# Kernel tuning notes

Hardware: AMD Instinct MI355X
Metric: run time of the kernel (lower is better)

Reference implementation:

```python
import jax, jax.numpy as jnp
import numpy as np

NUM_ITEM = 80000
NUM_USER = 20000
N = NUM_ITEM + NUM_USER
E = 1_000_000
DIM_FEAT = 64
USER_DIM = 128
DIM_ID = 64
SLOPE = 0.01  # F.leaky_relu default negative_slope


def setup_inputs() -> dict:
    key = jax.random.key(0)
    ks = jax.random.split(key, 16)
    s = 0.05
    # self-loop-free random edge list (torch code removes self loops)
    src = jax.random.randint(ks[0], (E,), 0, N)
    off = jax.random.randint(ks[1], (E,), 1, N)
    dst = (src + off) % N
    edge_index = jnp.stack([src, dst]).astype(jnp.int32)
    return {
        "features": jax.random.normal(ks[2], (NUM_ITEM, DIM_FEAT), jnp.float32),
        "user_features": jax.random.normal(ks[3], (NUM_USER, USER_DIM), jnp.float32),
        "id_embedding_weight": jax.random.normal(ks[4], (N, DIM_ID), jnp.float32) * s,
        "user_mlp_w": jax.random.normal(ks[5], (DIM_FEAT, USER_DIM), jnp.float32) * s,
        "user_mlp_b": jnp.zeros((DIM_FEAT,), jnp.float32),
        "gat1_w": jax.random.normal(ks[6], (DIM_FEAT, DIM_FEAT), jnp.float32) * s,
        "lin1_w": jax.random.normal(ks[7], (DIM_ID, DIM_FEAT), jnp.float32) * s,
        "lin1_b": jnp.zeros((DIM_ID,), jnp.float32),
        "g1_w": jax.random.normal(ks[8], (DIM_ID, DIM_FEAT), jnp.float32) * s,
        "g1_b": jnp.zeros((DIM_ID,), jnp.float32),
        "gat2_w": jax.random.normal(ks[9], (DIM_ID, DIM_ID), jnp.float32) * s,
        "lin2_w": jax.random.normal(ks[10], (DIM_ID, DIM_ID), jnp.float32) * s,
        "lin2_b": jnp.zeros((DIM_ID,), jnp.float32),
        "g2_w": jax.random.normal(ks[11], (DIM_ID, DIM_ID), jnp.float32) * s,
        "g2_b": jnp.zeros((DIM_ID,), jnp.float32),
        "edge_index": edge_index,
    }


def leaky_relu(x):
    return jnp.where(x >= 0, x, SLOPE * x)


def graph_gat(x, W, src, dst):
    """GraphGAT layer (MGAT-style): x@W, inner-product attention with
    degree-based sigmoid gate, edge softmax over target nodes, scatter-add."""
    n = x.shape[0]
    xw = x @ W                                   # [N, d_out]
    x_i = xw[dst]                                # gathered target feats [E, d]
    x_j = xw[src]                                # gathered source feats [E, d]
    inner = jnp.sum(x_i * x_j, axis=-1)          # [E]
    deg = jnp.zeros((n,), xw.dtype).at[src].add(1.0)
    dinv = deg[src] ** -0.5                      # deg[src] >= 1 by construction
    gate = jax.nn.sigmoid(dinv * inner)
    logits = inner * gate
    # segment softmax over destination index (PyG softmax)
    m = jax.ops.segment_max(logits, dst, num_segments=n)
    m = jnp.where(jnp.isfinite(m), m, 0.0)
    e = jnp.exp(logits - m[dst])
    z = jax.ops.segment_sum(e, dst, num_segments=n)
    attn = e / (z[dst] + 1e-16)
    msg = x_j * attn[:, None]                    # [E, d]
    return jnp.zeros_like(xw).at[dst].add(msg)   # scatter-add aggr


def reference(features, user_features, id_embedding_weight,
              user_mlp_w, user_mlp_b,
              gat1_w, lin1_w, lin1_b, g1_w, g1_b,
              gat2_w, lin2_w, lin2_b, g2_w, g2_b,
              edge_index):
    src, dst = edge_index[0], edge_index[1]
    user = jnp.tanh(user_features @ user_mlp_w.T + user_mlp_b)
    x = jnp.concatenate([features, user], axis=0)          # [N, dim_feat]
    nrm = jnp.linalg.norm(x, axis=-1, keepdims=True)
    x = x / jnp.maximum(nrm, 1e-12)                        # F.normalize

    # hop 1
    h = leaky_relu(graph_gat(x, gat1_w, src, dst))
    x_hat = leaky_relu(x @ lin1_w.T + lin1_b) + id_embedding_weight
    x1 = leaky_relu(h @ g1_w.T + g1_b + x_hat)

    # hop 2
    h = leaky_relu(graph_gat(x1, gat2_w, src, dst))
    x_hat = leaky_relu(x1 @ lin2_w.T + lin2_b) + id_embedding_weight
    x2 = leaky_relu(h @ g2_w.T + g2_b + x_hat)

    return jnp.concatenate([x1, x2], axis=1)               # [N, 2*dim_id]
```

## Files before the change

kernel.cpp:

```cpp
#include <hip/hip_runtime.h>
#include <hip/hip_bf16.h>

#define N_ITEM 80000
#define N_USER 20000
#define NN     100000
#define NE     1000000
#define SCAN_T 1024
#define SCAN_TILES ((NN + SCAN_T - 1) / SCAN_T)

typedef __hip_bfloat16 bf16;

__device__ __forceinline__ float b2f(bf16 v) { return __bfloat162float(v); }
__device__ __forceinline__ bf16  f2b(float v) { return __float2bfloat16(v); }
__device__ __forceinline__ float bits2f(unsigned short h) {
    return __uint_as_float(((unsigned)h) << 16);
}
__device__ __forceinline__ float leaky(float v) { return v >= 0.f ? v : 0.01f * v; }

template<typename T>
__device__ __forceinline__ float ldT(const void* p, size_t i);
template<> __device__ __forceinline__ float ldT<float>(const void* p, size_t i) {
    return ((const float*)p)[i];
}
template<> __device__ __forceinline__ float ldT<bf16>(const void* p, size_t i) {
    return b2f(((const bf16*)p)[i]);
}
template<typename T>
__device__ __forceinline__ float4 ldT4(const void* p, size_t i);
template<> __device__ __forceinline__ float4 ldT4<float>(const void* p, size_t i) {
    return *(const float4*)((const float*)p + i);
}
template<> __device__ __forceinline__ float4 ldT4<bf16>(const void* p, size_t i) {
    ushort4 u = *(const ushort4*)((const unsigned short*)p + i);
    return make_float4(bits2f(u.x), bits2f(u.y), bits2f(u.z), bits2f(u.w));
}
template<typename T>
__device__ __forceinline__ void stT4(void* p, size_t i, float4 v);
template<> __device__ __forceinline__ void stT4<float>(void* p, size_t i, float4 v) {
    *(float4*)((float*)p + i) = v;
}
template<> __device__ __forceinline__ void stT4<bf16>(void* p, size_t i, float4 v) {
    bf16 b0 = f2b(v.x), b1 = f2b(v.y), b2 = f2b(v.z), b3 = f2b(v.w);
    ushort4 u = make_ushort4(*(unsigned short*)&b0, *(unsigned short*)&b1,
                             *(unsigned short*)&b2, *(unsigned short*)&b3);
    *(ushort4*)((unsigned short*)p + i) = u;
}
__device__ __forceinline__ float4 ld4f(const float* p, size_t i) {
    return *(const float4*)(p + i);
}
__device__ __forceinline__ float4 ld4b(const unsigned short* p, size_t i) {
    ushort4 u = *(const ushort4*)(p + i);
    return make_float4(bits2f(u.x), bits2f(u.y), bits2f(u.z), bits2f(u.w));
}
__device__ __forceinline__ void st4b(unsigned short* p, size_t i, float4 v) {
    bf16 b0 = f2b(v.x), b1 = f2b(v.y), b2 = f2b(v.z), b3 = f2b(v.w);
    ushort4 u = make_ushort4(*(unsigned short*)&b0, *(unsigned short*)&b1,
                             *(unsigned short*)&b2, *(unsigned short*)&b3);
    *(ushort4*)(p + i) = u;
}

__device__ __forceinline__ float wred(float v) {
    for (int o = 32; o; o >>= 1) v += __shfl_xor(v, o, 64);
    return v;
}
__device__ __forceinline__ float gred16(float v) {
    for (int o = 8; o; o >>= 1) v += __shfl_xor(v, o, 64);
    return v;
}
__device__ __forceinline__ int wscan(int v, int lane) {
    for (int o = 1; o < 64; o <<= 1) {
        int t = __shfl_up(v, o, 64);
        v += (lane >= o) ? t : 0;
    }
    return v;
}

__global__ void k_detect(const unsigned short* __restrict__ w, int* __restrict__ mode) {
    __shared__ int cnt[256];
    int bad = 0;
    for (int i = threadIdx.x; i < 4096; i += 256) {
        unsigned e = (w[i] >> 7) & 0xFFu;
        bad += (e == 0u || e == 0xFFu) ? 1 : 0;
    }
    cnt[threadIdx.x] = bad;
    __syncthreads();
    if (threadIdx.x == 0) {
        int t = 0;
        for (int k = 0; k < 256; k++) t += cnt[k];
        mode[0] = (t > 0) ? 1 : 0;
    }
}

__global__ void k_prep_w(const void* umw, const void* lw1, const void* gw1,
                         const void* lw2, const void* gw2,
                         float* umwT, float* wT, const int* mode) {
    int t = blockIdx.x * 256 + threadIdx.x;
    bool f32m = (*mode != 0);
    if (t < 8192) {
        int j = t >> 7, k = t & 127;
        float v = f32m ? ldT<float>(umw, t) : ldT<bf16>(umw, t);
        umwT[k * 64 + j] = v;
    } else {
        int u = t - 8192;
        int m = u >> 12;
        int r = u & 4095;
        int j = r >> 6, k = r & 63;
        const void* srcp = (m == 0) ? lw1 : (m == 1) ? gw1 : (m == 2) ? lw2 : gw2;
        float v = f32m ? ldT<float>(srcp, r) : ldT<bf16>(srcp, r);
        wT[m * 4096 + k * 64 + j] = v;
    }
}

__global__ void k_deg(const int* __restrict__ src, const int* __restrict__ dst,
                      int* __restrict__ deg, int* __restrict__ cnt) {
    int e = blockIdx.x * blockDim.x + threadIdx.x;
    if (e < NE) {
        atomicAdd(&deg[src[e]], 1);
        atomicAdd(&cnt[dst[e]], 1);
    }
}

__global__ void k_dinv(const int* __restrict__ deg, float* __restrict__ dinv) {
    int i = blockIdx.x * blockDim.x + threadIdx.x;
    if (i < NN) dinv[i] = rsqrtf((float)max(deg[i], 1));
}

__global__ void k_scan_sum(const int* __restrict__ cnt, int* __restrict__ tsum) {
    __shared__ int wsum[16];
    int i = blockIdx.x * SCAN_T + threadIdx.x;
    int lane = threadIdx.x & 63, wid = threadIdx.x >> 6;
    int v = (i < NN) ? cnt[i] : 0;
    float s = wred((float)v);
    if (lane == 0) wsum[wid] = (int)s;
    __syncthreads();
    if (threadIdx.x == 0) {
        int t = 0;
        #pragma unroll
        for (int k = 0; k < 16; k++) t += wsum[k];
        tsum[blockIdx.x] = t;
    }
}

__global__ void k_scan_tiles(const int* __restrict__ tsum, int* __restrict__ toff) {
    __shared__ int wsum[16];
    int lane = threadIdx.x & 63, wid = threadIdx.x >> 6;
    int v = (threadIdx.x < SCAN_TILES) ? tsum[threadIdx.x] : 0;
    int inc = wscan(v, lane);
    if (lane == 63) wsum[wid] = inc;
    __syncthreads();
    if (wid == 0) {
        int ws = (lane < 16) ? wsum[lane] : 0;
        int wi = wscan(ws, lane);
        if (lane < 16) wsum[lane] = wi - ws;
    }
    __syncthreads();
    if (threadIdx.x < SCAN_TILES) toff[threadIdx.x] = inc - v + wsum[wid];
}

__global__ void k_scan_out(const int* __restrict__ cnt, const int* __restrict__ toff,
                           int* __restrict__ csr_off, int* __restrict__ cursor) {
    __shared__ int wsum[16];
    int i = blockIdx.x * SCAN_T + threadIdx.x;
    int lane = threadIdx.x & 63, wid = threadIdx.x >> 6;
    int v = (i < NN) ? cnt[i] : 0;
    int inc = wscan(v, lane);
    if (lane == 63) wsum[wid] = inc;
    __syncthreads();
    if (wid == 0) {
        int ws = (lane < 16) ? wsum[lane] : 0;
        int wi = wscan(ws, lane);
        if (lane < 16) wsum[lane] = wi - ws;
    }
    __syncthreads();
    int excl = inc - v + wsum[wid] + toff[blockIdx.x];
    if (i < NN) { csr_off[i] = excl; cursor[i] = excl; }
    if (i == NN - 1) csr_off[NN] = excl + v;
}

__global__ void k_scatter(const int* __restrict__ src, const int* __restrict__ dst,
                          int* __restrict__ cursor, int* __restrict__ csr_src) {
    int e = blockIdx.x * blockDim.x + threadIdx.x;
    if (e < NE) {
        int pos = atomicAdd(&cursor[dst[e]], 1);
        csr_src[pos] = src[e];
    }
}

template<typename T>
__device__ __forceinline__ void prep_items_body(const void* feat, float* x) {
    int i = blockIdx.x * 4 + (threadIdx.x >> 6);
    int j = threadIdx.x & 63;
    if (i >= N_ITEM) return;
    float v = ldT<T>(feat, (size_t)i * 64 + j);
    float ss = wred(v * v);
    float inv = 1.f / fmaxf(sqrtf(ss), 1e-12f);
    x[(size_t)i * 64 + j] = v * inv;
}
__global__ void k_prep_items(const void* feat, float* x, const int* mode) {
    if (*mode) prep_items_body<float>(feat, x);
    else       prep_items_body<bf16>(feat, x);
}

template<typename T>
__device__ __forceinline__ void prep_users_body(const void* uf, const float* wT,
                                                const void* b, float* x) {
    int u = blockIdx.x * 4 + (threadIdx.x >> 6);
    int j = threadIdx.x & 63;
    if (u >= N_USER) return;
    size_t ub = (size_t)u * 128;
    float acc = ldT<T>(b, j);
    #pragma unroll 8
    for (int k = 0; k < 128; k++)
        acc += ldT<T>(uf, ub + k) * wT[k * 64 + j];
    float v = tanhf(acc);
    float ss = wred(v * v);
    float inv = 1.f / fmaxf(sqrtf(ss), 1e-12f);
    x[(size_t)(N_ITEM + u) * 64 + j] = v * inv;
}
__global__ void k_prep_users(const void* uf, const float* wT, const void* b,
                             float* x, const int* mode) {
    if (*mode) prep_users_body<float>(uf, wT, b, x);
    else       prep_users_body<bf16>(uf, wT, b, x);
}

template<typename T>
__device__ __forceinline__ void xw_body(const float* __restrict__ xin,
                                        const void* __restrict__ W,
                                        unsigned short* __restrict__ xw) {
    int lane = threadIdx.x & 63, wid = threadIdx.x >> 6;
    int sl = lane & 15;
    int i = blockIdx.x * 16 + (wid << 2) + (lane >> 4);
    if (i >= NN) return;
    size_t rb = (size_t)i * 64 + sl * 4;
    float4 xv = ld4f(xin, rb);
    float4 acc = make_float4(0.f, 0.f, 0.f, 0.f);
    int gbase = lane & 48;
    #pragma unroll
    for (int kk = 0; kk < 16; kk++) {
        int srcl = gbase | kk;
        float xb[4];
        xb[0] = __shfl(xv.x, srcl, 64);
        xb[1] = __shfl(xv.y, srcl, 64);
        xb[2] = __shfl(xv.z, srcl, 64);
        xb[3] = __shfl(xv.w, srcl, 64);
        #pragma unroll
        for (int q = 0; q < 4; q++) {
            float4 w4 = ldT4<T>(W, (size_t)(kk * 4 + q) * 64 + sl * 4);
            acc.x += xb[q] * w4.x; acc.y += xb[q] * w4.y;
            acc.z += xb[q] * w4.z; acc.w += xb[q] * w4.w;
        }
    }
    st4b(xw, rb, acc);
}
__global__ void k_xw(const float* xin, const void* W, unsigned short* xw,
                     const int* mode) {
    if (*mode) xw_body<float>(xin, W, xw);
    else       xw_body<bf16>(xin, W, xw);
}

template<typename T>
__device__ __forceinline__ void gat_body(const unsigned short* __restrict__ xw,
                                         const float* __restrict__ xin,
                                         const int* __restrict__ csr_off,
                                         const int* __restrict__ csr_src,
                                         const float* __restrict__ dinv,
                                         const float* __restrict__ gT, const void* gb,
                                         const float* __restrict__ lT, const void* lb,
                                         const void* id_emb,
                                         float* __restrict__ xnext, void* out,
                                         int off_out) {
    int lane = threadIdx.x & 63, wid = threadIdx.x >> 6;
    int sl = lane & 15;
    int i = blockIdx.x * 16 + (wid << 2) + (lane >> 4);
    if (i >= NN) return;
    size_t rb = (size_t)i * 64 + sl * 4;
    float4 xd = ld4b(xw, rb);
    int e0 = csr_off[i], e1 = csr_off[i + 1];
    int cnt = e1 - e0;
    float m = -1e30f, l = 0.f;
    float4 acc = make_float4(0.f, 0.f, 0.f, 0.f);
    float4 xsA = make_float4(0.f, 0.f, 0.f, 0.f), xsB = xsA;
    float dA = 1.f, dB = 1.f;
    if (cnt > 0) {
        int s0 = csr_src[e0];
        xsA = ld4b(xw, (size_t)s0 * 64 + sl * 4);
        dA = dinv[s0];
    }
    if (cnt > 1) {
        int s1 = csr_src[e0 + 1];
        xsB = ld4b(xw, (size_t)s1 * 64 + sl * 4);
        dB = dinv[s1];
    }
    for (int t = 0; t < cnt; ++t) {
        float4 xs = xsA; float dv = dA;
        xsA = xsB; dA = dB;
        if (t + 2 < cnt) {
            int sn = csr_src[e0 + t + 2];
            xsB = ld4b(xw, (size_t)sn * 64 + sl * 4);
            dB = dinv[sn];
        }
        float p = xd.x * xs.x + xd.y * xs.y + xd.z * xs.z + xd.w * xs.w;
        float inner = gred16(p);
        float gate = 1.f / (1.f + __expf(-dv * inner));
        float logit = inner * gate;
        float mn = fmaxf(m, logit);
        float sc = __expf(m - mn);
        float w  = __expf(logit - mn);
        acc.x = acc.x * sc + w * xs.x;
        acc.y = acc.y * sc + w * xs.y;
        acc.z = acc.z * sc + w * xs.z;
        acc.w = acc.w * sc + w * xs.w;
        l = l * sc + w;
        m = mn;
    }
    float linv = 1.f / (l + 1e-16f);
    float4 hv = make_float4(leaky(acc.x * linv), leaky(acc.y * linv),
                            leaky(acc.z * linv), leaky(acc.w * linv));
    float4 xv = ld4f(xin, rb);
    float4 accg = make_float4(0.f, 0.f, 0.f, 0.f);
    float4 accl = make_float4(0.f, 0.f, 0.f, 0.f);
    int gbase = lane & 48;
    #pragma unroll
    for (int kk = 0; kk < 16; kk++) {
        int srcl = gbase | kk;
        float hb[4], xb[4];
        hb[0] = __shfl(hv.x, srcl, 64); xb[0] = __shfl(xv.x, srcl, 64);
        hb[1] = __shfl(hv.y, srcl, 64); xb[1] = __shfl(xv.y, srcl, 64);
        hb[2] = __shfl(hv.z, srcl, 64); xb[2] = __shfl(xv.z, srcl, 64);
        hb[3] = __shfl(hv.w, srcl, 64); xb[3] = __shfl(xv.w, srcl, 64);
        #pragma unroll
        for (int q = 0; q < 4; q++) {
            size_t wb = (size_t)(kk * 4 + q) * 64 + sl * 4;
            float4 g4 = ld4f(gT, wb);
            float4 l4 = ld4f(lT, wb);
            accg.x += hb[q] * g4.x; accg.y += hb[q] * g4.y;
            accg.z += hb[q] * g4.z; accg.w += hb[q] * g4.w;
            accl.x += xb[q] * l4.x; accl.y += xb[q] * l4.y;
            accl.z += xb[q] * l4.z; accl.w += xb[q] * l4.w;
        }
    }
    float4 lb4 = ldT4<T>(lb, sl * 4);
    float4 gb4 = ldT4<T>(gb, sl * 4);
    float4 id4 = ldT4<T>(id_emb, rb);
    float4 xn;
    xn.x = leaky(accg.x + gb4.x + leaky(accl.x + lb4.x) + id4.x);
    xn.y = leaky(accg.y + gb4.y + leaky(accl.y + lb4.y) + id4.y);
    xn.z = leaky(accg.z + gb4.z + leaky(accl.z + lb4.z) + id4.z);
    xn.w = leaky(accg.w + gb4.w + leaky(accl.w + lb4.w) + id4.w);
    *(float4*)(xnext + rb) = xn;
    stT4<T>(out, (size_t)i * 128 + off_out + sl * 4, xn);
}
__global__ void k_gat(const unsigned short* xw, const float* xin,
                      const int* csr_off, const int* csr_src, const float* dinv,
                      const float* gT, const void* gb,
                      const float* lT, const void* lb, const void* id_emb,
                      float* xnext, void* out, int off_out, const int* mode) {
    if (*mode) gat_body<float>(xw, xin, csr_off, csr_src, dinv, gT, gb, lT, lb,
                               id_emb, xnext, out, off_out);
    else       gat_body<bf16>(xw, xin, csr_off, csr_src, dinv, gT, gb, lT, lb,
                              id_emb, xnext, out, off_out);
}

extern "C" void kernel_launch(void* const* d_in, const int* in_sizes, int n_in,
                              void* d_out, int out_size, void* d_ws, size_t ws_size,
                              hipStream_t stream) {
    const void* feat   = d_in[0];
    const void* uf     = d_in[1];
    const void* id_emb = d_in[2];
    const void* umw    = d_in[3];
    const void* umb    = d_in[4];
    const void* gat1   = d_in[5];
    const void* lin1b  = d_in[7];
    const void* g1b    = d_in[9];
    const void* gat2   = d_in[10];
    const void* lin2b  = d_in[12];
    const void* g2b    = d_in[14];
    const int*  ei     = (const int*)d_in[15];
    const int* src = ei;
    const int* dst = ei + NE;

    int*      mode   = (int*)d_ws;
    int*      deg    = (int*)((char*)d_ws + 16);
    int*      cnt    = deg + NN;
    int*      cursor = cnt + NN;
    int*      csr_off = cursor + NN;
    int*      tsum   = csr_off + NN + 16;
    int*      toff   = tsum + 128;
    float*    dinv   = (float*)(toff + 128);
    float*    umwT   = dinv + NN;
    float*    wT     = umwT + 8192;
    int*      csr_src = (int*)(wT + 4 * 4096);
    float*    buf0   = (float*)(csr_src + NE);
    float*    buf2   = buf0 + (size_t)NN * 64;
    unsigned short* xwb = (unsigned short*)(buf2 + (size_t)NN * 64);

    k_detect<<<1, 256, 0, stream>>>((const unsigned short*)feat, mode);
    k_prep_w<<<96, 256, 0, stream>>>(umw, d_in[6], d_in[8], d_in[11], d_in[13],
                                     umwT, wT, mode);
    hipMemsetAsync(deg, 0, 2 * NN * 4, stream);
    k_deg<<<(NE + 255) / 256, 256, 0, stream>>>(src, dst, deg, cnt);
    k_dinv<<<(NN + 255) / 256, 256, 0, stream>>>(deg, dinv);
    k_scan_sum<<<SCAN_TILES, SCAN_T, 0, stream>>>(cnt, tsum);
    k_scan_tiles<<<1, SCAN_T, 0, stream>>>(tsum, toff);
    k_scan_out<<<SCAN_TILES, SCAN_T, 0, stream>>>(cnt, toff, csr_off, cursor);
    k_scatter<<<(NE + 255) / 256, 256, 0, stream>>>(src, dst, cursor, csr_src);
    k_prep_items<<<(N_ITEM + 3) / 4, 256, 0, stream>>>(feat, buf0, mode);
    k_prep_users<<<(N_USER + 3) / 4, 256, 0, stream>>>(uf, umwT, umb, buf0, mode);

    const float* lT1 = wT;
    const float* gT1 = wT + 4096;
    const float* lT2 = wT + 8192;
    const float* gT2 = wT + 12288;

    int gat_blocks = (NN + 15) / 16;

    k_xw<<<gat_blocks, 256, 0, stream>>>(buf0, gat1, xwb, mode);
    k_gat<<<gat_blocks, 256, 0, stream>>>(xwb, buf0, csr_off, csr_src, dinv,
                                          gT1, g1b, lT1, lin1b, id_emb,
                                          buf2, d_out, 0, mode);
    k_xw<<<gat_blocks, 256, 0, stream>>>(buf2, gat2, xwb, mode);
    k_gat<<<gat_blocks, 256, 0, stream>>>(xwb, buf2, csr_off, csr_src, dinv,
                                          gT2, g2b, lT2, lin2b, id_emb,
                                          buf0, d_out, 64, mode);
}
```

Before: 680.5 us.

## Drop online-softmax max tracking and prefetch four edges ahead in GAT gather

Replaces the online softmax (running max with rescaling) by direct exp-sum accumulation, which removes two exps and the rescale work per edge. It also deepens the software prefetch of neighbour features from two to four edges, keeping more gathers in flight. The trade-off is a risk of exp overflow if logits are large; with normalized inputs and small weights they are expected to stay bounded.

After: 699.6 us. 1.03x slower.

```diff
diff --git a/kernel.cpp b/kernel.cpp
--- a/kernel.cpp
+++ b/kernel.cpp
@@ -277,42 +277,42 @@
     float4 xd = ld4b(xw, rb);
     int e0 = csr_off[i], e1 = csr_off[i + 1];
     int cnt = e1 - e0;
-    float m = -1e30f, l = 0.f;
+    float l = 0.f;
     float4 acc = make_float4(0.f, 0.f, 0.f, 0.f);
-    float4 xsA = make_float4(0.f, 0.f, 0.f, 0.f), xsB = xsA;
-    float dA = 1.f, dB = 1.f;
-    if (cnt > 0) {
-        int s0 = csr_src[e0];
-        xsA = ld4b(xw, (size_t)s0 * 64 + sl * 4);
-        dA = dinv[s0];
-    }
-    if (cnt > 1) {
-        int s1 = csr_src[e0 + 1];
-        xsB = ld4b(xw, (size_t)s1 * 64 + sl * 4);
-        dB = dinv[s1];
-    }
-    for (int t = 0; t < cnt; ++t) {
-        float4 xs = xsA; float dv = dA;
-        xsA = xsB; dA = dB;
-        if (t + 2 < cnt) {
-            int sn = csr_src[e0 + t + 2];
-            xsB = ld4b(xw, (size_t)sn * 64 + sl * 4);
-            dB = dinv[sn];
-        }
-        float p = xd.x * xs.x + xd.y * xs.y + xd.z * xs.z + xd.w * xs.w;
-        float inner = gred16(p);
-        float gate = 1.f / (1.f + __expf(-dv * inner));
-        float logit = inner * gate;
-        float mn = fmaxf(m, logit);
-        float sc = __expf(m - mn);
-        float w  = __expf(logit - mn);
-        acc.x = acc.x * sc + w * xs.x;
-        acc.y = acc.y * sc + w * xs.y;
-        acc.z = acc.z * sc + w * xs.z;
-        acc.w = acc.w * sc + w * xs.w;
-        l = l * sc + w;
-        m = mn;
-    }
+
+    float4 xs0 = make_float4(0.f, 0.f, 0.f, 0.f);
+    float4 xs1 = xs0, xs2 = xs0, xs3 = xs0;
+    float d0v = 1.f, d1v = 1.f, d2v = 1.f, d3v = 1.f;
+
+#define LOADE(XS, DV, IDX) { int s_ = csr_src[e0 + (IDX)]; \
+        XS = ld4b(xw, (size_t)s_ * 64 + sl * 4); DV = dinv[s_]; }
+#define PROC(XS, DV) { \
+        float p_ = xd.x * XS.x + xd.y * XS.y + xd.z * XS.z + xd.w * XS.w; \
+        float inner_ = gred16(p_); \
+        float gate_ = 1.f / (1.f + __expf(-(DV) * inner_)); \
+        float w_ = __expf(inner_ * gate_); \
+        acc.x += w_ * XS.x; acc.y += w_ * XS.y; \
+        acc.z += w_ * XS.z; acc.w += w_ * XS.w; \
+        l += w_; }
+
+    if (cnt > 0) LOADE(xs0, d0v, 0);
+    if (cnt > 1) LOADE(xs1, d1v, 1);
+    if (cnt > 2) LOADE(xs2, d2v, 2);
+    if (cnt > 3) LOADE(xs3, d3v, 3);
+    int t = 0;
+    for (; t + 4 <= cnt; t += 4) {
+        PROC(xs0, d0v); if (t + 4 < cnt) LOADE(xs0, d0v, t + 4);
+        PROC(xs1, d1v); if (t + 5 < cnt) LOADE(xs1, d1v, t + 5);
+        PROC(xs2, d2v); if (t + 6 < cnt) LOADE(xs2, d2v, t + 6);
+        PROC(xs3, d3v); if (t + 7 < cnt) LOADE(xs3, d3v, t + 7);
+    }
+    if (t     < cnt) PROC(xs0, d0v);
+    if (t + 1 < cnt) PROC(xs1, d1v);
+    if (t + 2 < cnt) PROC(xs2, d2v);
+    if (t + 3 < cnt) PROC(xs3, d3v);
+#undef LOADE
+#undef PROC
+
     float linv = 1.f / (l + 1e-16f);
     float4 hv = make_float4(leaky(acc.x * linv), leaky(acc.y * linv),
                             leaky(acc.z * linv), leaky(acc.w * linv));
```

## Assign one wavefront per node and split edges across four lane groups

Applied to the files above, without the earlier changes.

The GAT aggregation now uses a full 64-lane wave per destination node, with four 16-lane groups processing different edges concurrently and combining partial sums via xor shuffles. The online-softmax max tracking is removed in favour of a direct exp-sum, and the dense g/lin projections are split across groups with a cross-group reduction. This shortens the serial per-node edge loop and reduces intra-wave divergence from uneven degrees, at the cost of 4x more waves, extra shuffle reductions, and loss of overflow protection in the softmax.

Result: slower. 778.1 us (+14.3%).

```diff
diff --git a/kernel.cpp b/kernel.cpp
--- a/kernel.cpp
+++ b/kernel.cpp
@@ -270,48 +270,55 @@
                                          float* __restrict__ xnext, void* out,
                                          int off_out) {
     int lane = threadIdx.x & 63, wid = threadIdx.x >> 6;
-    int sl = lane & 15;
-    int i = blockIdx.x * 16 + (wid << 2) + (lane >> 4);
+    int sl = lane & 15, sub = lane >> 4;
+    int i = blockIdx.x * 4 + wid;
     if (i >= NN) return;
     size_t rb = (size_t)i * 64 + sl * 4;
     float4 xd = ld4b(xw, rb);
     int e0 = csr_off[i], e1 = csr_off[i + 1];
     int cnt = e1 - e0;
-    float m = -1e30f, l = 0.f;
+    int nb = (cnt + 3) >> 2;
+    float l = 0.f;
     float4 acc = make_float4(0.f, 0.f, 0.f, 0.f);
+
     float4 xsA = make_float4(0.f, 0.f, 0.f, 0.f), xsB = xsA;
-    float dA = 1.f, dB = 1.f;
-    if (cnt > 0) {
-        int s0 = csr_src[e0];
-        xsA = ld4b(xw, (size_t)s0 * 64 + sl * 4);
-        dA = dinv[s0];
-    }
-    if (cnt > 1) {
-        int s1 = csr_src[e0 + 1];
-        xsB = ld4b(xw, (size_t)s1 * 64 + sl * 4);
-        dB = dinv[s1];
-    }
-    for (int t = 0; t < cnt; ++t) {
-        float4 xs = xsA; float dv = dA;
-        xsA = xsB; dA = dB;
-        if (t + 2 < cnt) {
-            int sn = csr_src[e0 + t + 2];
-            xsB = ld4b(xw, (size_t)sn * 64 + sl * 4);
-            dB = dinv[sn];
+    float dA = 1.f, dB = 1.f, aA = 0.f, aB = 0.f;
+    if (nb > 0) {
+        int q = sub;
+        int s_ = csr_src[e0 + min(q, cnt - 1)];
+        xsA = ld4b(xw, (size_t)s_ * 64 + sl * 4); dA = dinv[s_];
+        aA = (q < cnt) ? 1.f : 0.f;
+    }
+    if (nb > 1) {
+        int q = 4 + sub;
+        int s_ = csr_src[e0 + min(q, cnt - 1)];
+        xsB = ld4b(xw, (size_t)s_ * 64 + sl * 4); dB = dinv[s_];
+        aB = (q < cnt) ? 1.f : 0.f;
+    }
+    for (int b = 0; b < nb; ++b) {
+        float4 xs = xsA; float dv = dA; float am = aA;
+        xsA = xsB; dA = dB; aA = aB;
+        if (b + 2 < nb) {
+            int q = (b + 2) * 4 + sub;
+            int s_ = csr_src[e0 + min(q, cnt - 1)];
+            xsB = ld4b(xw, (size_t)s_ * 64 + sl * 4); dB = dinv[s_];
+            aB = (q < cnt) ? 1.f : 0.f;
         }
         float p = xd.x * xs.x + xd.y * xs.y + xd.z * xs.z + xd.w * xs.w;
         float inner = gred16(p);
         float gate = 1.f / (1.f + __expf(-dv * inner));
-        float logit = inner * gate;
-        float mn = fmaxf(m, logit);
-        float sc = __expf(m - mn);
-        float w  = __expf(logit - mn);
-        acc.x = acc.x * sc + w * xs.x;
-        acc.y = acc.y * sc + w * xs.y;
-        acc.z = acc.z * sc + w * xs.z;
-        acc.w = acc.w * sc + w * xs.w;
-        l = l * sc + w;
-        m = mn;
+        float w = am * __expf(inner * gate);
+        acc.x += w * xs.x; acc.y += w * xs.y;
+        acc.z += w * xs.z; acc.w += w * xs.w;
+        l += w;
+    }
+    #pragma unroll
+    for (int o = 16; o <= 32; o <<= 1) {
+        acc.x += __shfl_xor(acc.x, o, 64);
+        acc.y += __shfl_xor(acc.y, o, 64);
+        acc.z += __shfl_xor(acc.z, o, 64);
+        acc.w += __shfl_xor(acc.w, o, 64);
+        l     += __shfl_xor(l, o, 64);
     }
     float linv = 1.f / (l + 1e-16f);
     float4 hv = make_float4(leaky(acc.x * linv), leaky(acc.y * linv),
@@ -319,10 +326,11 @@
     float4 xv = ld4f(xin, rb);
     float4 accg = make_float4(0.f, 0.f, 0.f, 0.f);
     float4 accl = make_float4(0.f, 0.f, 0.f, 0.f);
-    int gbase = lane & 48;
+    int gb16 = lane & 48;
     #pragma unroll
-    for (int kk = 0; kk < 16; kk++) {
-        int srcl = gbase | kk;
+    for (int kt = 0; kt < 4; kt++) {
+        int kk = sub * 4 + kt;
+        int srcl = gb16 | kk;
         float hb[4], xb[4];
         hb[0] = __shfl(hv.x, srcl, 64); xb[0] = __shfl(xv.x, srcl, 64);
         hb[1] = __shfl(hv.y, srcl, 64); xb[1] = __shfl(xv.y, srcl, 64);
@@ -339,6 +347,17 @@
             accl.z += xb[q] * l4.z; accl.w += xb[q] * l4.w;
         }
     }
+    #pragma unroll
+    for (int o = 16; o <= 32; o <<= 1) {
+        accg.x += __shfl_xor(accg.x, o, 64);
+        accg.y += __shfl_xor(accg.y, o, 64);
+        accg.z += __shfl_xor(accg.z, o, 64);
+        accg.w += __shfl_xor(accg.w, o, 64);
+        accl.x += __shfl_xor(accl.x, o, 64);
+        accl.y += __shfl_xor(accl.y, o, 64);
+        accl.z += __shfl_xor(accl.z, o, 64);
+        accl.w += __shfl_xor(accl.w, o, 64);
+    }
     float4 lb4 = ldT4<T>(lb, sl * 4);
     float4 gb4 = ldT4<T>(gb, sl * 4);
     float4 id4 = ldT4<T>(id_emb, rb);
@@ -347,8 +366,8 @@
     xn.y = leaky(accg.y + gb4.y + leaky(accl.y + lb4.y) + id4.y);
     xn.z = leaky(accg.z + gb4.z + leaky(accl.z + lb4.z) + id4.z);
     xn.w = leaky(accg.w + gb4.w + leaky(accl.w + lb4.w) + id4.w);
-    *(float4*)(xnext + rb) = xn;
-    stT4<T>(out, (size_t)i * 128 + off_out + sl * 4, xn);
+    if (sub == 0) *(float4*)(xnext + rb) = xn;
+    if (sub == 1) stT4<T>(out, (size_t)i * 128 + off_out + sl * 4, xn);
 }
 __global__ void k_gat(const unsigned short* xw, const float* xin,
                       const int* csr_off, const int* csr_src, const float* dinv,
@@ -412,13 +431,14 @@
     const float* lT2 = wT + 8192;
     const float* gT2 = wT + 12288;
 
-    int gat_blocks = (NN + 15) / 16;
-
-    k_xw<<<gat_blocks, 256, 0, stream>>>(buf0, gat1, xwb, mode);
+    int xw_blocks  = (NN + 15) / 16;
+    int gat_blocks = (NN + 3) / 4;
+
+    k_xw<<<xw_blocks, 256, 0, stream>>>(buf0, gat1, xwb, mode);
     k_gat<<<gat_blocks, 256, 0, stream>>>(xwb, buf0, csr_off, csr_src, dinv,
                                           gT1, g1b, lT1, lin1b, id_emb,
                                           buf2, d_out, 0, mode);
-    k_xw<<<gat_blocks, 256, 0, stream>>>(buf2, gat2, xwb, mode);
+    k_xw<<<xw_blocks, 256, 0, stream>>>(buf2, gat2, xwb, mode);
     k_gat<<<gat_blocks, 256, 0, stream>>>(xwb, buf2, csr_off, csr_src, dinv,
                                           gT2, g2b, lT2, lin2b, id_emb,
                                           buf0, d_out, 64, mode);
```

## Move lin branch into pre-GAT kernel, cache g-weights in LDS, skip final xnext

Applied to the files above, without the earlier changes.

Moves the x@lin^T + bias + leaky + id_embedding computation out of the GAT aggregation kernel into the x@W kernel, which writes it as an fp16 intermediate. The GAT kernel then only does the g-projection, reading its 64x64 weight from shared memory loaded once per block. The second hop no longer writes the unused fp32 xnext buffer. The aim is to lighten the gather-bound GAT kernel and cut its global weight reads, at the cost of an extra fp16 round trip and some precision loss in x_hat.

Result: slower. 750.8 us (+10.3%).

```diff
diff --git a/kernel.cpp b/kernel.cpp
--- a/kernel.cpp
+++ b/kernel.cpp
@@ -1,5 +1,6 @@
 #include <hip/hip_runtime.h>
 #include <hip/hip_bf16.h>
+#include <hip/hip_fp16.h>
 
 #define N_ITEM 80000
 #define N_USER 20000
@@ -56,6 +57,21 @@
     bf16 b0 = f2b(v.x), b1 = f2b(v.y), b2 = f2b(v.z), b3 = f2b(v.w);
     ushort4 u = make_ushort4(*(unsigned short*)&b0, *(unsigned short*)&b1,
                              *(unsigned short*)&b2, *(unsigned short*)&b3);
+    *(ushort4*)(p + i) = u;
+}
+__device__ __forceinline__ float4 ld4h(const unsigned short* p, size_t i) {
+    ushort4 u = *(const ushort4*)(p + i);
+    __half h0, h1, h2, h3;
+    *(unsigned short*)&h0 = u.x; *(unsigned short*)&h1 = u.y;
+    *(unsigned short*)&h2 = u.z; *(unsigned short*)&h3 = u.w;
+    return make_float4(__half2float(h0), __half2float(h1),
+                       __half2float(h2), __half2float(h3));
+}
+__device__ __forceinline__ void st4h(unsigned short* p, size_t i, float4 v) {
+    __half h0 = __float2half(v.x), h1 = __float2half(v.y);
+    __half h2 = __float2half(v.z), h3 = __float2half(v.w);
+    ushort4 u = make_ushort4(*(unsigned short*)&h0, *(unsigned short*)&h1,
+                             *(unsigned short*)&h2, *(unsigned short*)&h3);
     *(ushort4*)(p + i) = u;
 }
 
@@ -224,16 +240,21 @@
 }
 
 template<typename T>
-__device__ __forceinline__ void xw_body(const float* __restrict__ xin,
-                                        const void* __restrict__ W,
-                                        unsigned short* __restrict__ xw) {
+__device__ __forceinline__ void pre_body(const float* __restrict__ xin,
+                                         const void* __restrict__ Wg,
+                                         const float* __restrict__ lT,
+                                         const void* __restrict__ lb,
+                                         const void* __restrict__ id_emb,
+                                         unsigned short* __restrict__ xw,
+                                         unsigned short* __restrict__ xhat) {
     int lane = threadIdx.x & 63, wid = threadIdx.x >> 6;
     int sl = lane & 15;
     int i = blockIdx.x * 16 + (wid << 2) + (lane >> 4);
     if (i >= NN) return;
     size_t rb = (size_t)i * 64 + sl * 4;
     float4 xv = ld4f(xin, rb);
-    float4 acc = make_float4(0.f, 0.f, 0.f, 0.f);
+    float4 accw = make_float4(0.f, 0.f, 0.f, 0.f);
+    float4 accl = make_float4(0.f, 0.f, 0.f, 0.f);
     int gbase = lane & 48;
     #pragma unroll
     for (int kk = 0; kk < 16; kk++) {
@@ -245,35 +266,51 @@
         xb[3] = __shfl(xv.w, srcl, 64);
         #pragma unroll
         for (int q = 0; q < 4; q++) {
-            float4 w4 = ldT4<T>(W, (size_t)(kk * 4 + q) * 64 + sl * 4);
-            acc.x += xb[q] * w4.x; acc.y += xb[q] * w4.y;
-            acc.z += xb[q] * w4.z; acc.w += xb[q] * w4.w;
+            size_t wb = (size_t)(kk * 4 + q) * 64 + sl * 4;
+            float4 w4 = ldT4<T>(Wg, wb);
+            float4 l4 = ld4f(lT, wb);
+            accw.x += xb[q] * w4.x; accw.y += xb[q] * w4.y;
+            accw.z += xb[q] * w4.z; accw.w += xb[q] * w4.w;
+            accl.x += xb[q] * l4.x; accl.y += xb[q] * l4.y;
+            accl.z += xb[q] * l4.z; accl.w += xb[q] * l4.w;
         }
     }
-    st4b(xw, rb, acc);
-}
-__global__ void k_xw(const float* xin, const void* W, unsigned short* xw,
-                     const int* mode) {
-    if (*mode) xw_body<float>(xin, W, xw);
-    else       xw_body<bf16>(xin, W, xw);
+    st4b(xw, rb, accw);
+    float4 lb4 = ldT4<T>(lb, sl * 4);
+    float4 id4 = ldT4<T>(id_emb, rb);
+    float4 xh;
+    xh.x = leaky(accl.x + lb4.x) + id4.x;
+    xh.y = leaky(accl.y + lb4.y) + id4.y;
+    xh.z = leaky(accl.z + lb4.z) + id4.z;
+    xh.w = leaky(accl.w + lb4.w) + id4.w;
+    st4h(xhat, rb, xh);
+}
+__global__ void k_pre(const float* xin, const void* Wg, const float* lT,
+                      const void* lb, const void* id_emb,
+                      unsigned short* xw, unsigned short* xhat, const int* mode) {
+    if (*mode) pre_body<float>(xin, Wg, lT, lb, id_emb, xw, xhat);
+    else       pre_body<bf16>(xin, Wg, lT, lb, id_emb, xw, xhat);
 }
 
 template<typename T>
 __device__ __forceinline__ void gat_body(const unsigned short* __restrict__ xw,
-                                         const float* __restrict__ xin,
+                                         const unsigned short* __restrict__ xhat,
                                          const int* __restrict__ csr_off,
                                          const int* __restrict__ csr_src,
                                          const float* __restrict__ dinv,
-                                         const float* __restrict__ gT, const void* gb,
-                                         const float* __restrict__ lT, const void* lb,
-                                         const void* id_emb,
+                                         const float* __restrict__ gTg,
+                                         const void* gb,
                                          float* __restrict__ xnext, void* out,
                                          int off_out) {
+    __shared__ float4 gs[1024];
     int lane = threadIdx.x & 63, wid = threadIdx.x >> 6;
     int sl = lane & 15;
     int i = blockIdx.x * 16 + (wid << 2) + (lane >> 4);
-    if (i >= NN) return;
     size_t rb = (size_t)i * 64 + sl * 4;
+    #pragma unroll
+    for (int t = 0; t < 4; t++)
+        gs[threadIdx.x + t * 256] = ((const float4*)gTg)[threadIdx.x + t * 256];
+
     float4 xd = ld4b(xw, rb);
     int e0 = csr_off[i], e1 = csr_off[i + 1];
     int cnt = e1 - e0;
@@ -316,49 +353,42 @@
     float linv = 1.f / (l + 1e-16f);
     float4 hv = make_float4(leaky(acc.x * linv), leaky(acc.y * linv),
                             leaky(acc.z * linv), leaky(acc.w * linv));
-    float4 xv = ld4f(xin, rb);
+    __syncthreads();
     float4 accg = make_float4(0.f, 0.f, 0.f, 0.f);
-    float4 accl = make_float4(0.f, 0.f, 0.f, 0.f);
     int gbase = lane & 48;
     #pragma unroll
     for (int kk = 0; kk < 16; kk++) {
         int srcl = gbase | kk;
-        float hb[4], xb[4];
-        hb[0] = __shfl(hv.x, srcl, 64); xb[0] = __shfl(xv.x, srcl, 64);
-        hb[1] = __shfl(hv.y, srcl, 64); xb[1] = __shfl(xv.y, srcl, 64);
-        hb[2] = __shfl(hv.z, srcl, 64); xb[2] = __shfl(xv.z, srcl, 64);
-        hb[3] = __shfl(hv.w, srcl, 64); xb[3] = __shfl(xv.w, srcl, 64);
+        float hb[4];
+        hb[0] = __shfl(hv.x, srcl, 64);
+        hb[1] = __shfl(hv.y, srcl, 64);
+        hb[2] = __shfl(hv.z, srcl, 64);
+        hb[3] = __shfl(hv.w, srcl, 64);
         #pragma unroll
         for (int q = 0; q < 4; q++) {
-            size_t wb = (size_t)(kk * 4 + q) * 64 + sl * 4;
-            float4 g4 = ld4f(gT, wb);
-            float4 l4 = ld4f(lT, wb);
+            float4 g4 = gs[(kk * 4 + q) * 16 + sl];
             accg.x += hb[q] * g4.x; accg.y += hb[q] * g4.y;
             accg.z += hb[q] * g4.z; accg.w += hb[q] * g4.w;
-            accl.x += xb[q] * l4.x; accl.y += xb[q] * l4.y;
-            accl.z += xb[q] * l4.z; accl.w += xb[q] * l4.w;
         }
     }
-    float4 lb4 = ldT4<T>(lb, sl * 4);
     float4 gb4 = ldT4<T>(gb, sl * 4);
-    float4 id4 = ldT4<T>(id_emb, rb);
+    float4 xh4 = ld4h(xhat, rb);
     float4 xn;
-    xn.x = leaky(accg.x + gb4.x + leaky(accl.x + lb4.x) + id4.x);
-    xn.y = leaky(accg.y + gb4.y + leaky(accl.y + lb4.y) + id4.y);
-    xn.z = leaky(accg.z + gb4.z + leaky(accl.z + lb4.z) + id4.z);
-    xn.w = leaky(accg.w + gb4.w + leaky(accl.w + lb4.w) + id4.w);
-    *(float4*)(xnext + rb) = xn;
+    xn.x = leaky(accg.x + gb4.x + xh4.x);
+    xn.y = leaky(accg.y + gb4.y + xh4.y);
+    xn.z = leaky(accg.z + gb4.z + xh4.z);
+    xn.w = leaky(accg.w + gb4.w + xh4.w);
+    if (xnext) *(float4*)(xnext + rb) = xn;
     stT4<T>(out, (size_t)i * 128 + off_out + sl * 4, xn);
 }
-__global__ void k_gat(const unsigned short* xw, const float* xin,
+__global__ void k_gat(const unsigned short* xw, const unsigned short* xhat,
                       const int* csr_off, const int* csr_src, const float* dinv,
-                      const float* gT, const void* gb,
-                      const float* lT, const void* lb, const void* id_emb,
+                      const float* gTg, const void* gb,
                       float* xnext, void* out, int off_out, const int* mode) {
-    if (*mode) gat_body<float>(xw, xin, csr_off, csr_src, dinv, gT, gb, lT, lb,
-                               id_emb, xnext, out, off_out);
-    else       gat_body<bf16>(xw, xin, csr_off, csr_src, dinv, gT, gb, lT, lb,
-                              id_emb, xnext, out, off_out);
+    if (*mode) gat_body<float>(xw, xhat, csr_off, csr_src, dinv, gTg, gb,
+                               xnext, out, off_out);
+    else       gat_body<bf16>(xw, xhat, csr_off, csr_src, dinv, gTg, gb,
+                              xnext, out, off_out);
 }
 
 extern "C" void kernel_launch(void* const* d_in, const int* in_sizes, int n_in,
@@ -392,7 +422,8 @@
     int*      csr_src = (int*)(wT + 4 * 4096);
     float*    buf0   = (float*)(csr_src + NE);
     float*    buf2   = buf0 + (size_t)NN * 64;
-    unsigned short* xwb = (unsigned short*)(buf2 + (size_t)NN * 64);
+    unsigned short* xwb   = (unsigned short*)(buf2 + (size_t)NN * 64);
+    unsigned short* xhath = xwb + (size_t)NN * 64;
 
     k_detect<<<1, 256, 0, stream>>>((const unsigned short*)feat, mode);
     k_prep_w<<<96, 256, 0, stream>>>(umw, d_in[6], d_in[8], d_in[11], d_in[13],
@@ -412,14 +443,14 @@
     const float* lT2 = wT + 8192;
     const float* gT2 = wT + 12288;
 
-    int gat_blocks = (NN + 15) / 16;
-
-    k_xw<<<gat_blocks, 256, 0, stream>>>(buf0, gat1, xwb, mode);
-    k_gat<<<gat_blocks, 256, 0, stream>>>(xwb, buf0, csr_off, csr_src, dinv,
-                                          gT1, g1b, lT1, lin1b, id_emb,
-                                          buf2, d_out, 0, mode);
-    k_xw<<<gat_blocks, 256, 0, stream>>>(buf2, gat2, xwb, mode);
-    k_gat<<<gat_blocks, 256, 0, stream>>>(xwb, buf2, csr_off, csr_src, dinv,
-                                          gT2, g2b, lT2, lin2b, id_emb,
-                                          buf0, d_out, 64, mode);
-}
+    int nb = NN / 16;
+
+    k_pre<<<nb, 256, 0, stream>>>(buf0, gat1, lT1, lin1b, id_emb,
+                                  xwb, xhath, mode);
+    k_gat<<<nb, 256, 0, stream>>>(xwb, xhath, csr_off, csr_src, dinv,
+                                  gT1, g1b, buf2, d_out, 0, mode);
+    k_pre<<<nb, 256, 0, stream>>>(buf2, gat2, lT2, lin2b, id_emb,
+                                  xwb, xhath, mode);
+    k_gat<<<nb, 256, 0, stream>>>(xwb, xhath, csr_off, csr_src, dinv,
+                                  gT2, g2b, nullptr, d_out, 64, mode);
+}
```
